# Kernel tuning notes

Measured on AMD Instinct MI355X. Metric: run time of the kernel, lower is better.

## Reference

```python
import jax, jax.numpy as jnp
import numpy as np
import math

B, S, D, H = 2, 2048, 1024, 16
DH = D // H
NEG = -1e9


def gelu(x):
    return 0.5 * x * (1.0 + jnp.tanh(math.sqrt(2.0 / math.pi) * (x + 0.044715 * x ** 3)))


def layernorm(x, g, b, eps=1e-6):
    # faithful to module: uses std (unbiased, N-1) and adds eps to std, not var
    mean = jnp.mean(x, axis=-1, keepdims=True)
    var = jnp.sum((x - mean) ** 2, axis=-1, keepdims=True) / (x.shape[-1] - 1)
    std = jnp.sqrt(var)
    return g * (x - mean) / (std + eps) + b


def setup_inputs() -> dict:
    key = jax.random.key(0)
    ks = jax.random.split(key, 13)
    sd = 0.02
    return {
        "x": jax.random.normal(ks[0], (B, S, D), jnp.float32),
        "w_attn": jax.random.normal(ks[1], (D, 3 * D), jnp.float32) * sd,
        "b_attn": jnp.zeros((3 * D,), jnp.float32),
        "w_aproj": jax.random.normal(ks[2], (D, D), jnp.float32) * sd,
        "b_aproj": jnp.zeros((D,), jnp.float32),
        "g1": jnp.ones((D,), jnp.float32),
        "b1": jnp.zeros((D,), jnp.float32),
        "w_fc": jax.random.normal(ks[3], (D, 4 * D), jnp.float32) * sd,
        "b_fc": jnp.zeros((4 * D,), jnp.float32),
        "w_mproj": jax.random.normal(ks[4], (4 * D, D), jnp.float32) * sd,
        "b_mproj": jnp.zeros((D,), jnp.float32),
        "g2": jnp.ones((D,), jnp.float32),
        "b2": jnp.zeros((D,), jnp.float32),
    }


def reference(x, w_attn, b_attn, w_aproj, b_aproj, g1, b1, w_fc, b_fc, w_mproj, b_mproj, g2, b2):
    # --- attention ---
    qkv = x @ w_attn + b_attn                       # [B,S,3D]
    q, k, v = jnp.split(qkv, 3, axis=2)
    q = q.reshape(B, S, H, DH).transpose(0, 2, 1, 3)  # [B,H,S,DH]
    k = k.reshape(B, S, H, DH).transpose(0, 2, 1, 3)
    v = v.reshape(B, S, H, DH).transpose(0, 2, 1, 3)
    w = jnp.einsum('bhqd,bhkd->bhqk', q, k) / math.sqrt(DH)
    mask = jnp.tril(jnp.ones((S, S), jnp.float32))[None, None]
    w = w * mask + NEG * (1.0 - mask)
    w = jax.nn.softmax(w, axis=-1)
    a = jnp.einsum('bhqk,bhkd->bhqd', w, v)         # [B,H,S,DH]
    a = a.transpose(0, 2, 1, 3).reshape(B, S, D)
    a = a @ w_aproj + b_aproj
    # --- postLN + MLP ---
    n = layernorm(x + a, g1, b1)
    h = gelu(n @ w_fc + b_fc)
    m = h @ w_mproj + b_mproj
    return layernorm(n + m, g2, b2)
```

## Files before the change

kernel.cpp:

```cpp
#include <hip/hip_runtime.h>
#include <type_traits>


typedef unsigned short u16;
typedef short s16x8 __attribute__((ext_vector_type(8)));
typedef unsigned short u16x4 __attribute__((ext_vector_type(4)));
typedef float f32x4 __attribute__((ext_vector_type(4)));
typedef float f32x16 __attribute__((ext_vector_type(16)));

__device__ __forceinline__ u16 f2b(float f) {
    union { float f; unsigned u; } x{f};
    unsigned r = x.u + 0x7FFFu + ((x.u >> 16) & 1u);
    return (u16)(r >> 16);
}

__device__ __forceinline__ float b2f(u16 v) {
    union { unsigned u; float f; } x;
    x.u = ((unsigned)v) << 16;
    return x.f;
}

__device__ __forceinline__ f32x4 mfma16(s16x8 a, s16x8 b, f32x4 c) {
    return __builtin_amdgcn_mfma_f32_16x16x32_bf16(a, b, c, 0, 0, 0);
}

__device__ __forceinline__ f32x16 mfma32(s16x8 a, s16x8 b, f32x16 c) {
    return __builtin_amdgcn_mfma_f32_32x32x16_bf16(a, b, c, 0, 0, 0);
}

__device__ __forceinline__ int cvtpk(float a, float b) {
    int r;
    asm("v_cvt_pk_bf16_f32 %0, %1, %2" : "=v"(r) : "v"(a), "v"(b));
    return r;
}

__device__ __forceinline__ void gld_lds16(const u16* g, u16* l) {
    __builtin_amdgcn_global_load_lds(
        (const __attribute__((address_space(1))) void*)g,
        (__attribute__((address_space(3))) void*)l, 16, 0, 0);
}

__global__ __launch_bounds__(256) void cvt_bf16(const float* __restrict__ in,
                                                u16* __restrict__ out, int n4) {
    int i = blockIdx.x * 256 + threadIdx.x;
    if (i < n4) {
        float4 v = ((const float4*)in)[i];
        u16x4 o = {f2b(v.x), f2b(v.y), f2b(v.z), f2b(v.w)};
        ((u16x4*)out)[i] = o;
    }
}

__global__ __launch_bounds__(256) void transpose_bf16(const float* __restrict__ W,
                                                      u16* __restrict__ WT,
                                                      int K, int N) {
    __shared__ float t[32][33];
    int tx = threadIdx.x & 31, ty = threadIdx.x >> 5;
    int n0 = blockIdx.x * 32, k0 = blockIdx.y * 32;
    #pragma unroll
    for (int r = ty; r < 32; r += 8)
        t[r][tx] = W[(size_t)(k0 + r) * N + n0 + tx];
    __syncthreads();
    #pragma unroll
    for (int r = ty; r < 32; r += 8)
        WT[(size_t)(n0 + r) * K + k0 + tx] = f2b(t[tx][r]);
}

template<int BN, bool GELU, typename OT>
__global__ __launch_bounds__(256) void gemm_db(const u16* __restrict__ A,
                                               const u16* __restrict__ BT,
                                               const float* __restrict__ bias,
                                               OT* __restrict__ C,
                                               int M, int N, int K, int ldc) {
    constexpr int NF = BN / 32;
    constexpr int BNI = BN / 32;
    __shared__ u16 As[2][128 * 64];
    __shared__ u16 Bs[2][BN * 64];

    int t = threadIdx.x;
    int w = t >> 6, l = t & 63, l16 = l & 15, lh = l >> 4;
    int wr = w >> 1, wc = w & 1;

    int nbm = M >> 7;
    int cpx = gridDim.x >> 3;
    int id = blockIdx.x;
    int id2 = (id & 7) * cpx + (id >> 3);
    size_t m0 = (size_t)(id2 % nbm) * 128;
    size_t n0 = (size_t)(id2 / nbm) * BN;

    int rowA = t >> 3;
    int gc = t & 7;
    int gc2 = gc ^ (((rowA >> 2) & 1) << 1) ^ (((rowA >> 3) & 1) << 2);
    const u16* Ag = A + (m0 + rowA) * (size_t)K + gc2 * 8;
    const u16* Bg = BT + (n0 + rowA) * (size_t)K + gc2 * 8;
    int wbase = w * 512;

    f32x4 acc[4][NF] = {};
    int cxor = (((l16 >> 2) & 1) << 4) ^ (((l16 >> 3) & 1) << 5);

    #pragma unroll
    for (int j = 0; j < 4; ++j)
        gld_lds16(Ag + (size_t)j * 32 * K, &As[0][j * 2048 + wbase]);
    #pragma unroll
    for (int j = 0; j < BNI; ++j)
        gld_lds16(Bg + (size_t)j * 32 * K, &Bs[0][j * 2048 + wbase]);
    __syncthreads();

    int cur = 0;
    for (int k0 = 0; k0 < K; k0 += 64) {
        if (k0 + 64 < K) {
            const u16* Ap = Ag + k0 + 64;
            #pragma unroll
            for (int j = 0; j < 4; ++j)
                gld_lds16(Ap + (size_t)j * 32 * K, &As[cur ^ 1][j * 2048 + wbase]);
            const u16* Bp = Bg + k0 + 64;
            #pragma unroll
            for (int j = 0; j < BNI; ++j)
                gld_lds16(Bp + (size_t)j * 32 * K, &Bs[cur ^ 1][j * 2048 + wbase]);
        }
        __builtin_amdgcn_s_setprio(1);
        #pragma unroll
        for (int ks = 0; ks < 2; ++ks) {
            s16x8 af[4], bf[NF];
            #pragma unroll
            for (int fm = 0; fm < 4; ++fm) {
                int row = wr * 64 + fm * 16 + l16;
                int col = (ks * 32 + lh * 8) ^ cxor;
                af[fm] = *(const s16x8*)&As[cur][row * 64 + col];
            }
            #pragma unroll
            for (int fn = 0; fn < NF; ++fn) {
                int row = wc * (BN / 2) + fn * 16 + l16;
                int col = (ks * 32 + lh * 8) ^ cxor;
                bf[fn] = *(const s16x8*)&Bs[cur][row * 64 + col];
            }
            #pragma unroll
            for (int fm = 0; fm < 4; ++fm)
                #pragma unroll
                for (int fn = 0; fn < NF; ++fn)
                    acc[fm][fn] = mfma16(af[fm], bf[fn], acc[fm][fn]);
        }
        __builtin_amdgcn_s_setprio(0);
        __syncthreads();
        cur ^= 1;
    }

    #pragma unroll
    for (int fn = 0; fn < NF; ++fn) {
        size_t col = n0 + wc * (BN / 2) + fn * 16 + l16;
        float bs = bias[col];
        #pragma unroll
        for (int fm = 0; fm < 4; ++fm) {
            size_t row0 = m0 + wr * 64 + fm * 16 + lh * 4;
            #pragma unroll
            for (int i = 0; i < 4; ++i) {
                float v = acc[fm][fn][i] + bs;
                if constexpr (GELU) {
                    float x3 = v * v * v;
                    v = 0.5f * v * (1.f + tanhf(0.7978845608f * (v + 0.044715f * x3)));
                }
                if constexpr (std::is_same<OT, u16>::value)
                    C[(row0 + i) * ldc + col] = f2b(v);
                else
                    C[(row0 + i) * ldc + col] = v;
            }
        }
    }
}

__global__ __launch_bounds__(256) void attn_kernel(const u16* __restrict__ qkv,
                                                   u16* __restrict__ p0,
                                                   u16* __restrict__ p1,
                                                   u16* __restrict__ p2,
                                                   float2* __restrict__ stats) {
    constexpr int S = 2048, D3 = 3072, Dm = 1024;
    __shared__ u16 Kl[2][64 * 64];
    __shared__ u16 Vt[2][64 * 64];

    int t = threadIdx.x;
    int w = t >> 6, l = t & 63;
    int l32 = l & 31, hi = l >> 5;
    int bid = blockIdx.x;
    int bh = bid & 31;
    int pr = (bid >> 5) & 7;
    int third = bid >> 8;
    int b = bh >> 4, h = bh & 15;
    size_t base = (size_t)b * S * D3;

    u16* pout = third == 0 ? p0 : (third == 1 ? p1 : p2);

    int rK0 = t >> 3, gK = t & 7;
    int rK1 = rK0 + 32;
    size_t koff0 = (size_t)rK0 * D3 + (size_t)((gK ^ (rK0 & 7)) * 8);
    size_t koff1 = (size_t)rK1 * D3 + (size_t)((gK ^ (rK1 & 7)) * 8);
    const u16* kbase = qkv + base + Dm + h * 64;
    const u16* vbase = qkv + base + 2 * Dm + h * 64 + w * 16;

    constexpr float cexp = 0.18033688011112042f;
    constexpr float THR = 64.0f;
    int xg = l32 & 7;

    #pragma unroll 1
    for (int ph = 0; ph < 2; ++ph) {
        int qt = ph ? (15 - pr) : pr;
        int qb = qt * 128 + w * 32;
        int nst = 2 * (qt + 1);
        int c0 = (nst * third) / 3;
        int c1 = (nst * (third + 1)) / 3;

        f32x16 O0 = {}, O1 = {};
        float m = -1e30f, lr = 0.f;

        if (c0 < c1) {
            s16x8 qf[4];
            const u16* qp = qkv + base + (size_t)(qb + l32) * D3 + h * 64 + hi * 8;
            #pragma unroll
            for (int kk = 0; kk < 4; ++kk)
                qf[kk] = *(const s16x8*)(qp + kk * 16);

            size_t kc0 = (size_t)c0 * 64 * D3;
            gld_lds16(kbase + kc0 + koff0, &Kl[0][w * 512]);
            gld_lds16(kbase + kc0 + koff1, &Kl[0][2048 + w * 512]);
            {
                const u16* vp = vbase + (size_t)(c0 * 64 + l) * D3;
                s16x8 pv0 = *(const s16x8*)vp;
                s16x8 pv1 = *(const s16x8*)(vp + 8);
                #pragma unroll
                for (int e = 0; e < 8; ++e) {
                    int d0 = w * 16 + e, d1 = w * 16 + 8 + e;
                    Vt[0][d0 * 64 + (l ^ ((d0 & 7) << 3))] = (u16)pv0[e];
                    Vt[0][d1 * 64 + (l ^ ((d1 & 7) << 3))] = (u16)pv1[e];
                }
            }
            __syncthreads();

            #pragma unroll 1
            for (int sc = c0; sc < c1; ++sc) {
                int cur = (sc - c0) & 1;
                bool pre = (sc + 1 < c1);
                s16x8 v0, v1;
                if (pre) {
                    size_t koffc = (size_t)(sc + 1) * 64 * D3;
                    gld_lds16(kbase + koffc + koff0, &Kl[cur ^ 1][w * 512]);
                    gld_lds16(kbase + koffc + koff1, &Kl[cur ^ 1][2048 + w * 512]);
                    const u16* vp = vbase + (size_t)((sc + 1) * 64 + l) * D3;
                    v0 = *(const s16x8*)vp;
                    v1 = *(const s16x8*)(vp + 8);
                }

                int kvb = sc * 64;
                int navail = ((qb - kvb) >> 5) + 1;
                if (navail > 0) {
                    if (navail > 2) navail = 2;
                    const u16* Kc = Kl[cur];
                    const u16* Vc = Vt[cur];
                    f32x16 sa0 = {}, sa1 = {};
                    #pragma unroll
                    for (int kk = 0; kk < 4; ++kk) {
                        s16x8 kf = *(const s16x8*)&Kc[l32 * 64 + (((2 * kk + hi) ^ xg) * 8)];
                        sa0 = mfma32(kf, qf[kk], sa0);
                    }
                    if (navail == 2) {
                        #pragma unroll
                        for (int kk = 0; kk < 4; ++kk) {
                            s16x8 kf = *(const s16x8*)&Kc[(32 + l32) * 64 + (((2 * kk + hi) ^ xg) * 8)];
                            sa1 = mfma32(kf, qf[kk], sa1);
                        }
                    }
                    bool diag0 = (kvb == qb);
                    bool diag1 = (kvb + 32 == qb);
                    float p[32];
                    float mx = -1e30f;
                    #pragma unroll
                    for (int reg = 0; reg < 16; ++reg) {
                        int kvloc = (reg & 3) + 8 * (reg >> 2) + 4 * hi;
                        float s0 = sa0[reg];
                        if (diag0 && kvloc > l32) s0 = -1e30f;
                        p[reg] = s0;
                        mx = fmaxf(mx, s0);
                    }
                    if (navail == 2) {
                        #pragma unroll
                        for (int reg = 0; reg < 16; ++reg) {
                            int kvloc = (reg & 3) + 8 * (reg >> 2) + 4 * hi;
                            float s1 = sa1[reg];
                            if (diag1 && kvloc > l32) s1 = -1e30f;
                            p[16 + reg] = s1;
                            mx = fmaxf(mx, s1);
                        }
                    }
                    mx = fmaxf(mx, __shfl_xor(mx, 32));
                    if (!__all(mx <= m + THR)) {
                        float mn = fmaxf(m, mx);
                        float a_ = exp2f(cexp * (m - mn));
                        m = mn;
                        #pragma unroll
                        for (int reg = 0; reg < 16; ++reg) {
                            int src = (reg & 3) + 8 * (reg >> 2) + 4 * hi;
                            float aq = __shfl(a_, src);
                            O0[reg] *= aq;
                            O1[reg] *= aq;
                        }
                        lr *= a_;
                    }
                    float rs = 0.f;
                    #pragma unroll
                    for (int reg = 0; reg < 16; ++reg) {
                        p[reg] = exp2f(cexp * (p[reg] - m));
                        rs += p[reg];
                    }
                    if (navail == 2) {
                        #pragma unroll
                        for (int reg = 16; reg < 32; ++reg) {
                            p[reg] = exp2f(cexp * (p[reg] - m));
                            rs += p[reg];
                        }
                    }
                    rs += __shfl_xor(rs, 32);
                    lr += rs;

                    #pragma unroll
                    for (int c = 0; c < 4; ++c) {
                        if (c < navail * 2) {
                            int pb = (c >> 1) * 16 + (c & 1) * 8;
                            int pk01 = cvtpk(p[pb + 0], p[pb + 1]);
                            int pk23 = cvtpk(p[pb + 2], p[pb + 3]);
                            int pk45 = cvtpk(p[pb + 4], p[pb + 5]);
                            int pk67 = cvtpk(p[pb + 6], p[pb + 7]);
                            int sx01 = __shfl_xor(pk01, 32);
                            int sx23 = __shfl_xor(pk23, 32);
                            int sx45 = __shfl_xor(pk45, 32);
                            int sx67 = __shfl_xor(pk67, 32);
                            union { int i[4]; s16x8 v; } u;
                            u.i[0] = hi ? sx45 : pk01;
                            u.i[1] = hi ? sx67 : pk23;
                            u.i[2] = hi ? pk45 : sx01;
                            u.i[3] = hi ? pk67 : sx23;
                            int go = ((c * 2 + hi) ^ xg) * 8;
                            s16x8 vb0 = *(const s16x8*)&Vc[l32 * 64 + go];
                            O0 = mfma32(u.v, vb0, O0);
                            s16x8 vb1 = *(const s16x8*)&Vc[(32 + l32) * 64 + go];
                            O1 = mfma32(u.v, vb1, O1);
                        }
                    }
                }

                if (pre) {
                    #pragma unroll
                    for (int e = 0; e < 8; ++e) {
                        int d0 = w * 16 + e, d1 = w * 16 + 8 + e;
                        Vt[cur ^ 1][d0 * 64 + (l ^ ((d0 & 7) << 3))] = (u16)v0[e];
                        Vt[cur ^ 1][d1 * 64 + (l ^ ((d1 & 7) << 3))] = (u16)v1[e];
                    }
                }
                __syncthreads();
            }
        }

        size_t obase = (size_t)b * S * 1024 + h * 64;
        #pragma unroll
        for (int reg = 0; reg < 16; ++reg) {
            int src = (reg & 3) + 8 * (reg >> 2) + 4 * hi;
            size_t row = obase + (size_t)(qb + src) * 1024;
            pout[row + l32] = f2b(O0[reg]);
            pout[row + 32 + l32] = f2b(O1[reg]);
        }
        if (hi == 0) {
            float2 st; st.x = m; st.y = lr;
            stats[third * 65536 + ((b * 2048 + qb + l32) * 16 + h)] = st;
        }
    }
}

__global__ __launch_bounds__(256) void merge_attn(u16* __restrict__ p0,
                                                  const u16* __restrict__ p1,
                                                  const u16* __restrict__ p2,
                                                  const float2* __restrict__ stats) {
    constexpr float cexp = 0.18033688011112042f;
    int gid = blockIdx.x * 256 + threadIdx.x;
    int rh = gid >> 2;
    int dc = (gid & 3) * 16;
    int R = rh >> 4, h = rh & 15;
    size_t addr = (size_t)R * 1024 + h * 64 + dc;

    float2 s0 = stats[rh];
    float2 s1 = stats[65536 + rh];
    float2 s2 = stats[131072 + rh];
    float M = fmaxf(s0.x, fmaxf(s1.x, s2.x));
    float a0 = exp2f(cexp * (s0.x - M));
    float a1 = exp2f(cexp * (s1.x - M));
    float a2 = exp2f(cexp * (s2.x - M));
    float inv = 1.f / (a0 * s0.y + a1 * s1.y + a2 * s2.y);
    a0 *= inv; a1 *= inv; a2 *= inv;

    u16x4 o[4];
    #pragma unroll
    for (int j = 0; j < 4; ++j) {
        u16x4 q0 = *(const u16x4*)(p0 + addr + j * 4);
        u16x4 q1 = *(const u16x4*)(p1 + addr + j * 4);
        u16x4 q2 = *(const u16x4*)(p2 + addr + j * 4);
        #pragma unroll
        for (int e = 0; e < 4; ++e)
            o[j][e] = f2b(a0 * b2f(q0[e]) + a1 * b2f(q1[e]) + a2 * b2f(q2[e]));
    }
    #pragma unroll
    for (int j = 0; j < 4; ++j)
        *(u16x4*)(p0 + addr + j * 4) = o[j];
}

template<bool WB>
__global__ __launch_bounds__(256) void resln(const float* __restrict__ xa,
                                             const float* __restrict__ xb2,
                                             const float* __restrict__ g,
                                             const float* __restrict__ be,
                                             float* __restrict__ outf,
                                             u16* __restrict__ outb) {
    int row = blockIdx.x;
    int t = threadIdx.x;
    size_t base = (size_t)row * 1024 + t * 4;
    float4 va = *(const float4*)(xa + base);
    float4 vb = *(const float4*)(xb2 + base);
    float v0 = va.x + vb.x, v1 = va.y + vb.y, v2 = va.z + vb.z, v3 = va.w + vb.w;
    float s1 = v0 + v1 + v2 + v3;
    float s2 = v0 * v0 + v1 * v1 + v2 * v2 + v3 * v3;
    #pragma unroll
    for (int off = 32; off >= 1; off >>= 1) {
        s1 += __shfl_down(s1, off);
        s2 += __shfl_down(s2, off);
    }
    __shared__ float r1[4], r2[4];
    if ((t & 63) == 0) { r1[t >> 6] = s1; r2[t >> 6] = s2; }
    __syncthreads();
    s1 = r1[0] + r1[1] + r1[2] + r1[3];
    s2 = r2[0] + r2[1] + r2[2] + r2[3];
    float mean = s1 * (1.f / 1024.f);
    float var = fmaxf((s2 - 1024.f * mean * mean) * (1.f / 1023.f), 0.f);
    float inv = 1.f / (sqrtf(var) + 1e-6f);
    int col = t * 4;
    float y0 = g[col + 0] * ((v0 - mean) * inv) + be[col + 0];
    float y1 = g[col + 1] * ((v1 - mean) * inv) + be[col + 1];
    float y2 = g[col + 2] * ((v2 - mean) * inv) + be[col + 2];
    float y3 = g[col + 3] * ((v3 - mean) * inv) + be[col + 3];
    float4 o = {y0, y1, y2, y3};
    *(float4*)(outf + base) = o;
    if constexpr (WB) {
        u16x4 ob = {f2b(y0), f2b(y1), f2b(y2), f2b(y3)};
        *(u16x4*)(outb + base) = ob;
    }
}

extern "C" void kernel_launch(void* const* d_in, const int* in_sizes, int n_in,
                              void* d_out, int out_size, void* d_ws, size_t ws_size,
                              hipStream_t stream) {
    (void)in_sizes; (void)n_in; (void)out_size; (void)ws_size;
    const float* x       = (const float*)d_in[0];
    const float* w_attn  = (const float*)d_in[1];
    const float* b_attn  = (const float*)d_in[2];
    const float* w_aproj = (const float*)d_in[3];
    const float* b_aproj = (const float*)d_in[4];
    const float* g1      = (const float*)d_in[5];
    const float* b1      = (const float*)d_in[6];
    const float* w_fc    = (const float*)d_in[7];
    const float* b_fc    = (const float*)d_in[8];
    const float* w_mproj = (const float*)d_in[9];
    const float* b_mproj = (const float*)d_in[10];
    const float* g2      = (const float*)d_in[11];
    const float* b2      = (const float*)d_in[12];
    float* out = (float*)d_out;

    constexpr int M = 4096;
    constexpr int D = 1024;

    char* ws = (char*)d_ws;
    u16*   slotA = (u16*)ws;
    char*  pB    = ws + (32u << 20);
    char*  pC    = ws + (40u << 20);
    char*  pD    = ws + (48u << 20);
    char*  pE    = ws + (64u << 20);

    u16*   xb    = (u16*)pB;
    u16*   wT    = (u16*)pC;
    u16*   qkv   = slotA;
    u16*   part0 = (u16*)pB;
    u16*   part1 = (u16*)pC;
    u16*   part2 = (u16*)pD;
    float2* stat = (float2*)pE;
    u16*   abuf  = (u16*)pB;
    float* aout  = (float*)pD;
    float* nbuf  = (float*)pE;
    u16*   nb    = (u16*)pB;
    u16*   h     = slotA;
    float* mout  = (float*)pD;

    dim3 blk(256);

    cvt_bf16<<<dim3(4096), blk, 0, stream>>>(x, xb, M * D / 4);

    transpose_bf16<<<dim3(3072 / 32, 1024 / 32), blk, 0, stream>>>(w_attn, wT, 1024, 3072);
    gemm_db<128, false, u16><<<dim3((M / 128) * (3072 / 128)), blk, 0, stream>>>(
        xb, wT, b_attn, qkv, M, 3072, 1024, 3072);

    attn_kernel<<<dim3(768), blk, 0, stream>>>(qkv, part0, part1, part2, stat);
    merge_attn<<<dim3(1024), blk, 0, stream>>>(part0, part1, part2, stat);

    transpose_bf16<<<dim3(1024 / 32, 1024 / 32), blk, 0, stream>>>(w_aproj, wT, 1024, 1024);
    gemm_db<64, false, float><<<dim3((M / 128) * (1024 / 64)), blk, 0, stream>>>(
        abuf, wT, b_aproj, aout, M, 1024, 1024, 1024);

    resln<true><<<dim3(M), blk, 0, stream>>>(x, aout, g1, b1, nbuf, nb);

    transpose_bf16<<<dim3(4096 / 32, 1024 / 32), blk, 0, stream>>>(w_fc, wT, 1024, 4096);
    gemm_db<128, true, u16><<<dim3((M / 128) * (4096 / 128)), blk, 0, stream>>>(
        nb, wT, b_fc, h, M, 4096, 1024, 4096);

    transpose_bf16<<<dim3(1024 / 32, 4096 / 32), blk, 0, stream>>>(w_mproj, wT, 4096, 1024);
    gemm_db<64, false, float><<<dim3((M / 128) * (1024 / 64)), blk, 0, stream>>>(
        h, wT, b_mproj, mout, M, 1024, 4096, 1024);

    resln<false><<<dim3(M), blk, 0, stream>>>(nbuf, mout, g2, b2, out, nullptr);
}
```

Baseline: 302.8 us.

## Replace double-buffered GEMM with single-buffered LDS and full XOR swizzle

Drops LDS double buffering in the bf16 GEMM, so each K step now loads its tile, synchronizes, computes, then synchronizes again. It also removes the s_setprio hints and replaces the partial two-bit swizzle with a full (row&7) XOR swizzle to cut LDS bank conflicts. Halving LDS use allows more resident blocks per CU, which may hide latency through occupancy, but global-to-LDS loads no longer overlap with MFMA work inside a block.

```diff
diff --git a/kernel.cpp b/kernel.cpp
--- a/kernel.cpp
+++ b/kernel.cpp
@@ -66,15 +66,15 @@
 }
 
 template<int BN, bool GELU, typename OT>
-__global__ __launch_bounds__(256) void gemm_db(const u16* __restrict__ A,
+__global__ __launch_bounds__(256) void gemm_sb(const u16* __restrict__ A,
                                                const u16* __restrict__ BT,
                                                const float* __restrict__ bias,
                                                OT* __restrict__ C,
                                                int M, int N, int K, int ldc) {
     constexpr int NF = BN / 32;
     constexpr int BNI = BN / 32;
-    __shared__ u16 As[2][128 * 64];
-    __shared__ u16 Bs[2][BN * 64];
+    __shared__ u16 As[128 * 64];
+    __shared__ u16 Bs[BN * 64];
 
     int t = threadIdx.x;
     int w = t >> 6, l = t & 63, l16 = l & 15, lh = l >> 4;
@@ -88,50 +88,37 @@
     size_t n0 = (size_t)(id2 / nbm) * BN;
 
     int rowA = t >> 3;
-    int gc = t & 7;
-    int gc2 = gc ^ (((rowA >> 2) & 1) << 1) ^ (((rowA >> 3) & 1) << 2);
+    int gc2 = (t & 7) ^ (rowA & 7);
     const u16* Ag = A + (m0 + rowA) * (size_t)K + gc2 * 8;
     const u16* Bg = BT + (n0 + rowA) * (size_t)K + gc2 * 8;
     int wbase = w * 512;
 
     f32x4 acc[4][NF] = {};
-    int cxor = (((l16 >> 2) & 1) << 4) ^ (((l16 >> 3) & 1) << 5);
-
-    #pragma unroll
-    for (int j = 0; j < 4; ++j)
-        gld_lds16(Ag + (size_t)j * 32 * K, &As[0][j * 2048 + wbase]);
-    #pragma unroll
-    for (int j = 0; j < BNI; ++j)
-        gld_lds16(Bg + (size_t)j * 32 * K, &Bs[0][j * 2048 + wbase]);
-    __syncthreads();
-
-    int cur = 0;
+    int rx = (l16 & 7) * 8;
+
     for (int k0 = 0; k0 < K; k0 += 64) {
-        if (k0 + 64 < K) {
-            const u16* Ap = Ag + k0 + 64;
-            #pragma unroll
-            for (int j = 0; j < 4; ++j)
-                gld_lds16(Ap + (size_t)j * 32 * K, &As[cur ^ 1][j * 2048 + wbase]);
-            const u16* Bp = Bg + k0 + 64;
-            #pragma unroll
-            for (int j = 0; j < BNI; ++j)
-                gld_lds16(Bp + (size_t)j * 32 * K, &Bs[cur ^ 1][j * 2048 + wbase]);
-        }
-        __builtin_amdgcn_s_setprio(1);
+        #pragma unroll
+        for (int j = 0; j < 4; ++j)
+            gld_lds16(Ag + k0 + (size_t)j * 32 * K, &As[j * 2048 + wbase]);
+        #pragma unroll
+        for (int j = 0; j < BNI; ++j)
+            gld_lds16(Bg + k0 + (size_t)j * 32 * K, &Bs[j * 2048 + wbase]);
+        __syncthreads();
+
         #pragma unroll
         for (int ks = 0; ks < 2; ++ks) {
             s16x8 af[4], bf[NF];
             #pragma unroll
             for (int fm = 0; fm < 4; ++fm) {
                 int row = wr * 64 + fm * 16 + l16;
-                int col = (ks * 32 + lh * 8) ^ cxor;
-                af[fm] = *(const s16x8*)&As[cur][row * 64 + col];
+                int col = ((ks * 4 + lh) * 8) ^ rx;
+                af[fm] = *(const s16x8*)&As[row * 64 + col];
             }
             #pragma unroll
             for (int fn = 0; fn < NF; ++fn) {
                 int row = wc * (BN / 2) + fn * 16 + l16;
-                int col = (ks * 32 + lh * 8) ^ cxor;
-                bf[fn] = *(const s16x8*)&Bs[cur][row * 64 + col];
+                int col = ((ks * 4 + lh) * 8) ^ rx;
+                bf[fn] = *(const s16x8*)&Bs[row * 64 + col];
             }
             #pragma unroll
             for (int fm = 0; fm < 4; ++fm)
@@ -139,9 +126,7 @@
                 for (int fn = 0; fn < NF; ++fn)
                     acc[fm][fn] = mfma16(af[fm], bf[fn], acc[fm][fn]);
         }
-        __builtin_amdgcn_s_setprio(0);
         __syncthreads();
-        cur ^= 1;
     }
 
     #pragma unroll
@@ -496,24 +481,24 @@
     cvt_bf16<<<dim3(4096), blk, 0, stream>>>(x, xb, M * D / 4);
 
     transpose_bf16<<<dim3(3072 / 32, 1024 / 32), blk, 0, stream>>>(w_attn, wT, 1024, 3072);
-    gemm_db<128, false, u16><<<dim3((M / 128) * (3072 / 128)), blk, 0, stream>>>(
+    gemm_sb<128, false, u16><<<dim3((M / 128) * (3072 / 128)), blk, 0, stream>>>(
         xb, wT, b_attn, qkv, M, 3072, 1024, 3072);
 
     attn_kernel<<<dim3(768), blk, 0, stream>>>(qkv, part0, part1, part2, stat);
     merge_attn<<<dim3(1024), blk, 0, stream>>>(part0, part1, part2, stat);
 
     transpose_bf16<<<dim3(1024 / 32, 1024 / 32), blk, 0, stream>>>(w_aproj, wT, 1024, 1024);
-    gemm_db<64, false, float><<<dim3((M / 128) * (1024 / 64)), blk, 0, stream>>>(
+    gemm_sb<64, false, float><<<dim3((M / 128) * (1024 / 64)), blk, 0, stream>>>(
         abuf, wT, b_aproj, aout, M, 1024, 1024, 1024);
 
     resln<true><<<dim3(M), blk, 0, stream>>>(x, aout, g1, b1, nbuf, nb);
 
     transpose_bf16<<<dim3(4096 / 32, 1024 / 32), blk, 0, stream>>>(w_fc, wT, 1024, 4096);
-    gemm_db<128, true, u16><<<dim3((M / 128) * (4096 / 128)), blk, 0, stream>>>(
+    gemm_sb<128, true, u16><<<dim3((M / 128) * (4096 / 128)), blk, 0, stream>>>(
         nb, wT, b_fc, h, M, 4096, 1024, 4096);
 
     transpose_bf16<<<dim3(1024 / 32, 4096 / 32), blk, 0, stream>>>(w_mproj, wT, 4096, 1024);
-    gemm_db<64, false, float><<<dim3((M / 128) * (1024 / 64)), blk, 0, stream>>>(
+    gemm_sb<64, false, float><<<dim3((M / 128) * (1024 / 64)), blk, 0, stream>>>(
         h, wT, b_mproj, mout, M, 1024, 4096, 1024);
 
     resln<false><<<dim3(M), blk, 0, stream>>>(nbuf, mout, g2, b2, out, nullptr);
```

After: 308.6 us. No clear change (+1.9%).
